# Kernel tuning notes

Hardware: AMD Instinct MI355X
Metric: run time of the kernel (lower is better)

## Reference

```python
import jax, jax.numpy as jnp
import numpy as np

B = 4096
SEQ = 128            # window_size * rnn_in_pkts
WINDOW = 32
IN_PKTS = 4
LEN_V, LEN_E = 1500, 64
IPD_V, IPD_E = 256, 64
EV = 64              # embedding_vector_bits
RNN_IN = IN_PKTS * EV   # 256
H = 256              # rnn_hidden_bits
LABELS = 100


def setup_inputs() -> dict:
    key = jax.random.key(0)
    ks = jax.random.split(key, 12)
    s = 0.05
    return {
        "len_x": jax.random.randint(ks[0], (B, SEQ), 0, LEN_V),
        "ipd_x": jax.random.randint(ks[1], (B, SEQ), 0, IPD_V),
        "len_emb": jax.random.normal(ks[2], (LEN_V, LEN_E), jnp.float32) * s,
        "ipd_emb": jax.random.normal(ks[3], (IPD_V, IPD_E), jnp.float32) * s,
        "fc_w": jax.random.normal(ks[4], (EV, LEN_E + IPD_E), jnp.float32) * s,
        "fc_b": jax.random.normal(ks[5], (EV,), jnp.float32) * s,
        "w_ih": jax.random.normal(ks[6], (3 * H, RNN_IN), jnp.float32) * s,
        "w_hh": jax.random.normal(ks[7], (3 * H, H), jnp.float32) * s,
        "b_ih": jax.random.normal(ks[8], (3 * H,), jnp.float32) * s,
        "b_hh": jax.random.normal(ks[9], (3 * H,), jnp.float32) * s,
        "out_w": jax.random.normal(ks[10], (LABELS, H), jnp.float32) * s,
        "out_b": jax.random.normal(ks[11], (LABELS,), jnp.float32) * s,
    }


def _gru_scan(rnn_in, w_ih, w_hh, b_ih, b_hh):
    # rnn_in: [B, T, RNN_IN]. Precompute input-side gates for all steps at once.
    gi_all = jnp.einsum("bti,gi->btg", rnn_in, w_ih) + b_ih  # [B,T,3H]
    h0 = jnp.zeros((rnn_in.shape[0], H), rnn_in.dtype)

    def step(h, gi):
        gh = h @ w_hh.T + b_hh                 # [B,3H]
        i_r, i_z, i_n = jnp.split(gi, 3, axis=-1)
        h_r, h_z, h_n = jnp.split(gh, 3, axis=-1)
        r = jax.nn.sigmoid(i_r + h_r)
        z = jax.nn.sigmoid(i_z + h_z)
        n = jnp.tanh(i_n + r * h_n)
        h_new = (1.0 - z) * n + z * h
        return h_new, None

    h_final, _ = jax.lax.scan(step, h0, jnp.swapaxes(gi_all, 0, 1))
    return h_final


def reference(len_x, ipd_x, len_emb, ipd_emb, fc_w, fc_b, w_ih, w_hh, b_ih, b_hh, out_w, out_b):
    len_e = len_emb[len_x]                      # [B,SEQ,LEN_E]
    ipd_e = ipd_emb[ipd_x]                      # [B,SEQ,IPD_E]
    cat = jnp.concatenate([len_e, ipd_e], axis=-1)
    evs = cat @ fc_w.T + fc_b                   # [B,SEQ,EV]
    rnn_in = evs.reshape(B, WINDOW, RNN_IN)     # [B,32,256]
    h = _gru_scan(rnn_in, w_ih, w_hh, b_ih, b_hh)
    logits = h @ out_w.T + out_b                # [B,LABELS]
    return logits
```

## Files before the change

kernel.cpp:

```cpp
#include <hip/hip_runtime.h>
#include <hip/hip_bf16.h>

typedef __bf16 bf16_t;
typedef __bf16 bf16x8 __attribute__((ext_vector_type(8)));
typedef float f32x4 __attribute__((ext_vector_type(4)));
typedef unsigned short u16x4 __attribute__((ext_vector_type(4)));

#define MFMA16(a, b, c) __builtin_amdgcn_mfma_f32_16x16x32_bf16((a), (b), (c), 0, 0, 0)

#define BATCH 4096
#define SEQN 128
#define HN 256
#define NLABELS 100
#define TSTEPS 32
#define LEN_VN 1500
#define IPD_VN 256

#define OFF_LENT   0u
#define OFF_IPDT   384000u
#define OFF_WIH    449536u
#define OFF_WHH    842752u
#define OFF_GI     1235968u
#define WS_NEEDED  202562560u

__device__ __forceinline__ float sigf(float x) {
    return __builtin_amdgcn_rcpf(1.f + __expf(-x));
}
__device__ __forceinline__ float tanh_fast(float x) {
    return 2.f * __builtin_amdgcn_rcpf(1.f + __expf(-2.f * x)) - 1.f;
}
__device__ __forceinline__ float b2f(unsigned short v) {
    union { unsigned u; float f; } c; c.u = ((unsigned)v) << 16; return c.f;
}
__device__ __forceinline__ unsigned short f2b(float f) {
    union { bf16_t h; unsigned short s; } c; c.h = (bf16_t)f; return c.s;
}

__device__ __forceinline__ void barrier_lds() {
    asm volatile("s_waitcnt lgkmcnt(0)\n\ts_barrier" ::: "memory");
}

__global__ void prep_kernel(const float* __restrict__ len_emb,
                            const float* __restrict__ ipd_emb,
                            const float* __restrict__ fc_w,
                            const float* __restrict__ fc_b,
                            const float* __restrict__ w_ih,
                            const float* __restrict__ w_hh,
                            float* __restrict__ lenT, float* __restrict__ ipdT,
                            bf16_t* __restrict__ wfrag_ih,
                            bf16_t* __restrict__ wfrag_hh) {
    const int bid = blockIdx.x, tid = threadIdx.x;
    if (bid < 439) {
        const int row = bid * 4 + (tid >> 6);
        const int e = tid & 63;
        if (row < LEN_VN) {
            const float* emb = len_emb + row * 64;
            const float* wv = fc_w + e * 128;
            float s = fc_b[e];
            #pragma unroll 8
            for (int j = 0; j < 64; ++j) s += emb[j] * wv[j];
            lenT[row * 64 + e] = s;
        } else if (row < LEN_VN + IPD_VN) {
            const int v = row - LEN_VN;
            const float* emb = ipd_emb + v * 64;
            const float* wv = fc_w + e * 128 + 64;
            float s = 0.f;
            #pragma unroll 8
            for (int j = 0; j < 64; ++j) s += emb[j] * wv[j];
            ipdT[v * 64 + e] = s;
        }
    } else {
        const int flat = (bid - 439) * 256 + tid;
        const int which = flat / 24576;
        const int rem = flat % 24576;
        const int c = rem >> 9;
        const int kt = (rem >> 6) & 7;
        const int lane = rem & 63;
        const int g = c * 16 + (lane & 15);
        const int k0 = kt * 32 + (lane >> 4) * 8;
        const float* src = (which == 0 ? w_ih : w_hh) + g * 256 + k0;
        bf16_t* dst = (which == 0 ? wfrag_ih : wfrag_hh) + ((c * 8 + kt) * 64 + lane) * 8;
        f32x4 s0 = *(const f32x4*)(src);
        f32x4 s1 = *(const f32x4*)(src + 4);
        bf16x8 o;
        #pragma unroll
        for (int j = 0; j < 4; ++j) { o[j] = (bf16_t)s0[j]; o[4 + j] = (bf16_t)s1[j]; }
        *(bf16x8*)dst = o;
    }
}

__global__ void __launch_bounds__(1024, 4)
gemm_gi(const int* __restrict__ len_x, const int* __restrict__ ipd_x,
        const float* __restrict__ lenT, const float* __restrict__ ipdT,
        const bf16_t* __restrict__ wfrag_ih,
        const float* __restrict__ b_ih, const float* __restrict__ b_hh,
        bf16_t* __restrict__ gi) {
    __shared__ bf16_t wlds[16 * 8 * 512];
    __shared__ bf16_t a_lds[2][8 * 512];

    const int tid = threadIdx.x;
    const int lane = tid & 63;
    const int w = tid >> 6;
    const int bt = blockIdx.x;
    const int col = lane & 15;

    bf16x8 wr[2][8];
    #pragma unroll
    for (int cc = 0; cc < 2; ++cc) {
        const int ct = cc * 16 + w;
        #pragma unroll
        for (int kt = 0; kt < 8; ++kt)
            wr[cc][kt] = *(const bf16x8*)(wfrag_ih + ((ct * 8 + kt) * 64 + lane) * 8);
    }
    #pragma unroll
    for (int kt = 0; kt < 8; ++kt)
        *(bf16x8*)&wlds[(w * 8 + kt) * 512 + lane * 8] =
            *(const bf16x8*)(wfrag_ih + (((32 + w) * 8 + kt) * 64 + lane) * 8);

    float bias0 = b_ih[w * 16 + col] + b_hh[w * 16 + col];
    float bias1 = b_ih[256 + w * 16 + col] + b_hh[256 + w * 16 + col];
    float bias2 = b_ih[512 + w * 16 + col];

    const int b_row = bt * 16 + (lane & 15);
    const int gkt = (tid >> 6) & 7;
    const int k0 = gkt * 32 + (lane >> 4) * 8;
    const int p = k0 >> 6;
    const int e0 = k0 & 63;

    auto do_gather = [&](int t) {
        const int seq = t * 4 + p;
        const int v1 = len_x[b_row * SEQN + seq];
        const int v2 = ipd_x[b_row * SEQN + seq];
        const f32x4* lp = (const f32x4*)(lenT + v1 * 64 + e0);
        const f32x4* ip = (const f32x4*)(ipdT + v2 * 64 + e0);
        f32x4 a0 = lp[0] + ip[0];
        f32x4 a1 = lp[1] + ip[1];
        bf16x8 o;
        #pragma unroll
        for (int j = 0; j < 4; ++j) { o[j] = (bf16_t)a0[j]; o[4 + j] = (bf16_t)a1[j]; }
        *(bf16x8*)&a_lds[t & 1][gkt * 512 + lane * 8] = o;
    };

    if (tid < 512) do_gather(0);
    bf16_t* gib = gi + (size_t)bt * 48 * 32 * 256 + lane * 4;
    const bf16_t* wb = &wlds[w * 8 * 512 + lane * 8];

    for (int t = 0; t < TSTEPS; ++t) {
        barrier_lds();
        if (t + 1 < TSTEPS && tid < 512) do_gather(t + 1);

        f32x4 acc0 = {}, acc1 = {}, acc2 = {};
        const bf16_t* ab = &a_lds[t & 1][lane * 8];
        #pragma unroll
        for (int kt = 0; kt < 8; ++kt) {
            bf16x8 af = *(const bf16x8*)(ab + kt * 512);
            bf16x8 w5 = *(const bf16x8*)(wb + kt * 512);
            acc0 = MFMA16(af, wr[0][kt], acc0);
            acc1 = MFMA16(af, wr[1][kt], acc1);
            acc2 = MFMA16(af, w5, acc2);
        }

        u16x4 o0, o1, o2;
        #pragma unroll
        for (int r = 0; r < 4; ++r) {
            o0[r] = f2b(acc0[r] + bias0);
            o1[r] = f2b(acc1[r] + bias1);
            o2[r] = f2b(acc2[r] + bias2);
        }
        *(u16x4*)(gib + ((size_t)(w) * 32 + t) * 256) = o0;
        *(u16x4*)(gib + ((size_t)(16 + w) * 32 + t) * 256) = o1;
        *(u16x4*)(gib + ((size_t)(32 + w) * 32 + t) * 256) = o2;
    }
}

__global__ void __launch_bounds__(1024, 4)
gru_kernel(const bf16_t* __restrict__ gi,
           const bf16_t* __restrict__ wfrag_hh,
           const float* __restrict__ b_hh,
           const float* __restrict__ out_w,
           const float* __restrict__ out_b,
           float* __restrict__ out) {
    __shared__ char smem[147456];
    bf16_t* wlds = (bf16_t*)smem;
    bf16_t* h_lds = (bf16_t*)(smem + 131072);
    float* h_fin = (float*)smem;

    const int tid = threadIdx.x;
    const int lane = tid & 63;
    const int w = tid >> 6;
    const int bt = blockIdx.x;
    const int col = lane & 15;
    const int j = w * 16 + col;

    bf16x8 wr[2][8];
    #pragma unroll
    for (int cc = 0; cc < 2; ++cc) {
        const int ct = cc * 16 + w;
        #pragma unroll
        for (int kt = 0; kt < 8; ++kt)
            wr[cc][kt] = *(const bf16x8*)(wfrag_hh + ((ct * 8 + kt) * 64 + lane) * 8);
    }
    #pragma unroll
    for (int kt = 0; kt < 8; ++kt)
        *(bf16x8*)&wlds[(w * 8 + kt) * 512 + lane * 8] =
            *(const bf16x8*)(wfrag_hh + (((32 + w) * 8 + kt) * 64 + lane) * 8);

    const float b_hn = b_hh[512 + j];

    for (int i = tid; i < 4096; i += 1024) h_lds[4096 + i] = (bf16_t)0.f;

    const int woff = (j >> 5) * 512 + (((j >> 3) & 3) * 16 + (lane >> 4) * 4) * 8 + (j & 7);

    f32x4 hprev = {};
    const bf16_t* gib = gi + (size_t)bt * 48 * 32 * 256 + lane * 4;
    const bf16_t* wb = &wlds[w * 8 * 512 + lane * 8];

    for (int t = 0; t < TSTEPS; ++t) {
        barrier_lds();

        u16x4 g0 = *(const u16x4*)(gib + ((size_t)(w) * 32 + t) * 256);
        u16x4 g1 = *(const u16x4*)(gib + ((size_t)(16 + w) * 32 + t) * 256);
        u16x4 g2 = *(const u16x4*)(gib + ((size_t)(32 + w) * 32 + t) * 256);

        const bf16_t* hb = &h_lds[((t + 1) & 1) * 4096 + lane * 8];
        f32x4 acc0 = {}, acc1 = {}, acc2 = {};
        #pragma unroll
        for (int kt = 0; kt < 8; ++kt) {
            bf16x8 ah = *(const bf16x8*)(hb + kt * 512);
            bf16x8 w5 = *(const bf16x8*)(wb + kt * 512);
            acc0 = MFMA16(ah, wr[0][kt], acc0);
            acc1 = MFMA16(ah, wr[1][kt], acc1);
            acc2 = MFMA16(ah, w5, acc2);
        }

        bf16_t* hw = &h_lds[(t & 1) * 4096 + woff];
        #pragma unroll
        for (int r = 0; r < 4; ++r) {
            float rg = sigf(acc0[r] + b2f(g0[r]));
            float zg = sigf(acc1[r] + b2f(g1[r]));
            float ng = tanh_fast(b2f(g2[r]) + rg * (acc2[r] + b_hn));
            float hn = ng + zg * (hprev[r] - ng);
            hprev[r] = hn;
            hw[r * 8] = (bf16_t)hn;
        }
    }

    __syncthreads();

    #pragma unroll
    for (int r = 0; r < 4; ++r) {
        const int m = (lane >> 4) * 4 + r;
        h_fin[m * 260 + j] = hprev[r];
    }
    __syncthreads();

    for (int i = tid; i < 16 * NLABELS; i += 1024) {
        const int row = i / NLABELS;
        const int cl = i - row * NLABELS;
        const f32x4* wrow = (const f32x4*)(out_w + cl * 256);
        const f32x4* hr = (const f32x4*)(h_fin + row * 260);
        f32x4 acc = {0.f, 0.f, 0.f, 0.f};
        #pragma unroll 4
        for (int k = 0; k < 64; ++k) acc += hr[k] * wrow[k];
        out[(bt * 16 + row) * NLABELS + cl] =
            out_b[cl] + acc[0] + acc[1] + acc[2] + acc[3];
    }
}

extern "C" void kernel_launch(void* const* d_in, const int* in_sizes, int n_in,
                              void* d_out, int out_size, void* d_ws, size_t ws_size,
                              hipStream_t stream) {
    (void)in_sizes; (void)n_in; (void)out_size; (void)ws_size;
    const int*   len_x   = (const int*)d_in[0];
    const int*   ipd_x   = (const int*)d_in[1];
    const float* len_emb = (const float*)d_in[2];
    const float* ipd_emb = (const float*)d_in[3];
    const float* fc_w    = (const float*)d_in[4];
    const float* fc_b    = (const float*)d_in[5];
    const float* w_ih    = (const float*)d_in[6];
    const float* w_hh    = (const float*)d_in[7];
    const float* b_ih    = (const float*)d_in[8];
    const float* b_hh    = (const float*)d_in[9];
    const float* out_w   = (const float*)d_in[10];
    const float* out_b   = (const float*)d_in[11];

    char* ws = (char*)d_ws;
    float*  lenT = (float*)(ws + OFF_LENT);
    float*  ipdT = (float*)(ws + OFF_IPDT);
    bf16_t* wfi  = (bf16_t*)(ws + OFF_WIH);
    bf16_t* wfh  = (bf16_t*)(ws + OFF_WHH);
    bf16_t* gi   = (bf16_t*)(ws + OFF_GI);

    prep_kernel<<<631, 256, 0, stream>>>(len_emb, ipd_emb, fc_w, fc_b,
                                         w_ih, w_hh, lenT, ipdT, wfi, wfh);
    gemm_gi<<<256, 1024, 0, stream>>>(len_x, ipd_x, lenT, ipdT, wfi,
                                      b_ih, b_hh, gi);
    gru_kernel<<<256, 1024, 0, stream>>>(gi, wfh, b_hh, out_w, out_b,
                                         (float*)d_out);
}
```

Baseline: 249.7 us.

## Halve block size, give each wave two column tiles per gate

Both the input-gate GEMM and the GRU recurrence kernels now launch 512-thread blocks instead of 1024. Each wave owns two 16-column tiles per gate, six accumulators in total, with five tiles held in registers and one in LDS. The MFMA operands are swapped so the weights act as the A operand, which yields a transposed output layout. Hidden-state writes and biases become vectorized 4-wide. The intent is to cut LDS footprint and per-step barrier cost across fewer waves while raising MFMA work per wave, at the price of much higher register pressure.

New measurement: 263.9 us. 1.06x slower.

```diff
diff --git a/kernel.cpp b/kernel.cpp
--- a/kernel.cpp
+++ b/kernel.cpp
@@ -89,41 +89,44 @@
     }
 }
 
-__global__ void __launch_bounds__(1024, 4)
+__global__ void __launch_bounds__(512, 2)
 gemm_gi(const int* __restrict__ len_x, const int* __restrict__ ipd_x,
         const float* __restrict__ lenT, const float* __restrict__ ipdT,
         const bf16_t* __restrict__ wfrag_ih,
         const float* __restrict__ b_ih, const float* __restrict__ b_hh,
         bf16_t* __restrict__ gi) {
-    __shared__ bf16_t wlds[16 * 8 * 512];
+    __shared__ bf16_t wlds[8 * 8 * 512];
     __shared__ bf16_t a_lds[2][8 * 512];
 
     const int tid = threadIdx.x;
     const int lane = tid & 63;
     const int w = tid >> 6;
     const int bt = blockIdx.x;
-    const int col = lane & 15;
-
-    bf16x8 wr[2][8];
-    #pragma unroll
-    for (int cc = 0; cc < 2; ++cc) {
-        const int ct = cc * 16 + w;
+    const int quad = lane >> 4;
+
+    const int cts[6] = {2*w, 2*w + 1, 16 + 2*w, 17 + 2*w, 32 + 2*w, 33 + 2*w};
+
+    bf16x8 wr[5][8];
+    #pragma unroll
+    for (int cc = 0; cc < 5; ++cc)
         #pragma unroll
         for (int kt = 0; kt < 8; ++kt)
-            wr[cc][kt] = *(const bf16x8*)(wfrag_ih + ((ct * 8 + kt) * 64 + lane) * 8);
-    }
+            wr[cc][kt] = *(const bf16x8*)(wfrag_ih + ((cts[cc] * 8 + kt) * 64 + lane) * 8);
     #pragma unroll
     for (int kt = 0; kt < 8; ++kt)
         *(bf16x8*)&wlds[(w * 8 + kt) * 512 + lane * 8] =
-            *(const bf16x8*)(wfrag_ih + (((32 + w) * 8 + kt) * 64 + lane) * 8);
-
-    float bias0 = b_ih[w * 16 + col] + b_hh[w * 16 + col];
-    float bias1 = b_ih[256 + w * 16 + col] + b_hh[256 + w * 16 + col];
-    float bias2 = b_ih[512 + w * 16 + col];
+            *(const bf16x8*)(wfrag_ih + ((cts[5] * 8 + kt) * 64 + lane) * 8);
+
+    f32x4 bias[6];
+    #pragma unroll
+    for (int cc = 0; cc < 6; ++cc) {
+        f32x4 v = *(const f32x4*)(b_ih + cts[cc] * 16 + quad * 4);
+        if (cc < 4) v += *(const f32x4*)(b_hh + cts[cc] * 16 + quad * 4);
+        bias[cc] = v;
+    }
 
     const int b_row = bt * 16 + (lane & 15);
-    const int gkt = (tid >> 6) & 7;
-    const int k0 = gkt * 32 + (lane >> 4) * 8;
+    const int k0 = w * 32 + quad * 8;
     const int p = k0 >> 6;
     const int e0 = k0 & 63;
 
@@ -138,123 +141,135 @@
         bf16x8 o;
         #pragma unroll
         for (int j = 0; j < 4; ++j) { o[j] = (bf16_t)a0[j]; o[4 + j] = (bf16_t)a1[j]; }
-        *(bf16x8*)&a_lds[t & 1][gkt * 512 + lane * 8] = o;
+        *(bf16x8*)&a_lds[t & 1][w * 512 + lane * 8] = o;
     };
 
-    if (tid < 512) do_gather(0);
+    do_gather(0);
     bf16_t* gib = gi + (size_t)bt * 48 * 32 * 256 + lane * 4;
     const bf16_t* wb = &wlds[w * 8 * 512 + lane * 8];
 
     for (int t = 0; t < TSTEPS; ++t) {
         barrier_lds();
-        if (t + 1 < TSTEPS && tid < 512) do_gather(t + 1);
-
-        f32x4 acc0 = {}, acc1 = {}, acc2 = {};
+        if (t + 1 < TSTEPS) do_gather(t + 1);
+
+        f32x4 acc[6] = {};
         const bf16_t* ab = &a_lds[t & 1][lane * 8];
         #pragma unroll
         for (int kt = 0; kt < 8; ++kt) {
-            bf16x8 af = *(const bf16x8*)(ab + kt * 512);
+            bf16x8 xf = *(const bf16x8*)(ab + kt * 512);
             bf16x8 w5 = *(const bf16x8*)(wb + kt * 512);
-            acc0 = MFMA16(af, wr[0][kt], acc0);
-            acc1 = MFMA16(af, wr[1][kt], acc1);
-            acc2 = MFMA16(af, w5, acc2);
-        }
-
-        u16x4 o0, o1, o2;
-        #pragma unroll
-        for (int r = 0; r < 4; ++r) {
-            o0[r] = f2b(acc0[r] + bias0);
-            o1[r] = f2b(acc1[r] + bias1);
-            o2[r] = f2b(acc2[r] + bias2);
-        }
-        *(u16x4*)(gib + ((size_t)(w) * 32 + t) * 256) = o0;
-        *(u16x4*)(gib + ((size_t)(16 + w) * 32 + t) * 256) = o1;
-        *(u16x4*)(gib + ((size_t)(32 + w) * 32 + t) * 256) = o2;
-    }
-}
-
-__global__ void __launch_bounds__(1024, 4)
+            acc[0] = MFMA16(wr[0][kt], xf, acc[0]);
+            acc[1] = MFMA16(wr[1][kt], xf, acc[1]);
+            acc[2] = MFMA16(wr[2][kt], xf, acc[2]);
+            acc[3] = MFMA16(wr[3][kt], xf, acc[3]);
+            acc[4] = MFMA16(wr[4][kt], xf, acc[4]);
+            acc[5] = MFMA16(w5, xf, acc[5]);
+        }
+
+        #pragma unroll
+        for (int cc = 0; cc < 6; ++cc) {
+            u16x4 o;
+            #pragma unroll
+            for (int r = 0; r < 4; ++r) o[r] = f2b(acc[cc][r] + bias[cc][r]);
+            *(u16x4*)(gib + ((size_t)cts[cc] * 32 + t) * 256) = o;
+        }
+    }
+}
+
+__global__ void __launch_bounds__(512, 2)
 gru_kernel(const bf16_t* __restrict__ gi,
            const bf16_t* __restrict__ wfrag_hh,
            const float* __restrict__ b_hh,
            const float* __restrict__ out_w,
            const float* __restrict__ out_b,
            float* __restrict__ out) {
-    __shared__ char smem[147456];
+    __shared__ char smem[81920];
     bf16_t* wlds = (bf16_t*)smem;
-    bf16_t* h_lds = (bf16_t*)(smem + 131072);
+    bf16_t* h_lds = (bf16_t*)(smem + 65536);
     float* h_fin = (float*)smem;
 
     const int tid = threadIdx.x;
     const int lane = tid & 63;
     const int w = tid >> 6;
     const int bt = blockIdx.x;
-    const int col = lane & 15;
-    const int j = w * 16 + col;
-
-    bf16x8 wr[2][8];
-    #pragma unroll
-    for (int cc = 0; cc < 2; ++cc) {
-        const int ct = cc * 16 + w;
+    const int quad = lane >> 4;
+    const int b = lane & 15;
+
+    const int cts[6] = {2*w, 2*w + 1, 16 + 2*w, 17 + 2*w, 32 + 2*w, 33 + 2*w};
+
+    bf16x8 wr[5][8];
+    #pragma unroll
+    for (int cc = 0; cc < 5; ++cc)
         #pragma unroll
         for (int kt = 0; kt < 8; ++kt)
-            wr[cc][kt] = *(const bf16x8*)(wfrag_hh + ((ct * 8 + kt) * 64 + lane) * 8);
-    }
+            wr[cc][kt] = *(const bf16x8*)(wfrag_hh + ((cts[cc] * 8 + kt) * 64 + lane) * 8);
     #pragma unroll
     for (int kt = 0; kt < 8; ++kt)
         *(bf16x8*)&wlds[(w * 8 + kt) * 512 + lane * 8] =
-            *(const bf16x8*)(wfrag_hh + (((32 + w) * 8 + kt) * 64 + lane) * 8);
-
-    const float b_hn = b_hh[512 + j];
-
-    for (int i = tid; i < 4096; i += 1024) h_lds[4096 + i] = (bf16_t)0.f;
-
-    const int woff = (j >> 5) * 512 + (((j >> 3) & 3) * 16 + (lane >> 4) * 4) * 8 + (j & 7);
-
-    f32x4 hprev = {};
+            *(const bf16x8*)(wfrag_hh + ((cts[5] * 8 + kt) * 64 + lane) * 8);
+
+    f32x4 bhn[2];
+    bhn[0] = *(const f32x4*)(b_hh + cts[4] * 16 + quad * 4);
+    bhn[1] = *(const f32x4*)(b_hh + cts[5] * 16 + quad * 4);
+
+    for (int i = tid; i < 4096; i += 512) h_lds[4096 + i] = (bf16_t)0.f;
+
+    int woff[2];
+    #pragma unroll
+    for (int s = 0; s < 2; ++s)
+        woff[s] = w * 512 + (((2 * s + (quad >> 1)) & 3) * 16 + b) * 8 + 4 * (quad & 1);
+
+    f32x4 hprev[2] = {};
     const bf16_t* gib = gi + (size_t)bt * 48 * 32 * 256 + lane * 4;
     const bf16_t* wb = &wlds[w * 8 * 512 + lane * 8];
 
     for (int t = 0; t < TSTEPS; ++t) {
         barrier_lds();
 
-        u16x4 g0 = *(const u16x4*)(gib + ((size_t)(w) * 32 + t) * 256);
-        u16x4 g1 = *(const u16x4*)(gib + ((size_t)(16 + w) * 32 + t) * 256);
-        u16x4 g2 = *(const u16x4*)(gib + ((size_t)(32 + w) * 32 + t) * 256);
+        u16x4 g[6];
+        #pragma unroll
+        for (int cc = 0; cc < 6; ++cc)
+            g[cc] = *(const u16x4*)(gib + ((size_t)cts[cc] * 32 + t) * 256);
 
         const bf16_t* hb = &h_lds[((t + 1) & 1) * 4096 + lane * 8];
-        f32x4 acc0 = {}, acc1 = {}, acc2 = {};
+        f32x4 acc[6] = {};
         #pragma unroll
         for (int kt = 0; kt < 8; ++kt) {
-            bf16x8 ah = *(const bf16x8*)(hb + kt * 512);
+            bf16x8 hf = *(const bf16x8*)(hb + kt * 512);
             bf16x8 w5 = *(const bf16x8*)(wb + kt * 512);
-            acc0 = MFMA16(ah, wr[0][kt], acc0);
-            acc1 = MFMA16(ah, wr[1][kt], acc1);
-            acc2 = MFMA16(ah, w5, acc2);
-        }
-
-        bf16_t* hw = &h_lds[(t & 1) * 4096 + woff];
-        #pragma unroll
-        for (int r = 0; r < 4; ++r) {
-            float rg = sigf(acc0[r] + b2f(g0[r]));
-            float zg = sigf(acc1[r] + b2f(g1[r]));
-            float ng = tanh_fast(b2f(g2[r]) + rg * (acc2[r] + b_hn));
-            float hn = ng + zg * (hprev[r] - ng);
-            hprev[r] = hn;
-            hw[r * 8] = (bf16_t)hn;
+            acc[0] = MFMA16(wr[0][kt], hf, acc[0]);
+            acc[1] = MFMA16(wr[1][kt], hf, acc[1]);
+            acc[2] = MFMA16(wr[2][kt], hf, acc[2]);
+            acc[3] = MFMA16(wr[3][kt], hf, acc[3]);
+            acc[4] = MFMA16(wr[4][kt], hf, acc[4]);
+            acc[5] = MFMA16(w5, hf, acc[5]);
+        }
+
+        bf16_t* hwb = &h_lds[(t & 1) * 4096];
+        #pragma unroll
+        for (int s = 0; s < 2; ++s) {
+            u16x4 o;
+            #pragma unroll
+            for (int r = 0; r < 4; ++r) {
+                float rg = sigf(acc[s][r] + b2f(g[s][r]));
+                float zg = sigf(acc[2 + s][r] + b2f(g[2 + s][r]));
+                float ng = tanh_fast(b2f(g[4 + s][r]) + rg * (acc[4 + s][r] + bhn[s][r]));
+                float hn = ng + zg * (hprev[s][r] - ng);
+                hprev[s][r] = hn;
+                o[r] = f2b(hn);
+            }
+            *(u16x4*)(hwb + woff[s]) = o;
         }
     }
 
     __syncthreads();
 
     #pragma unroll
-    for (int r = 0; r < 4; ++r) {
-        const int m = (lane >> 4) * 4 + r;
-        h_fin[m * 260 + j] = hprev[r];
-    }
+    for (int s = 0; s < 2; ++s)
+        *(f32x4*)(h_fin + b * 260 + 32 * w + 16 * s + 4 * quad) = hprev[s];
     __syncthreads();
 
-    for (int i = tid; i < 16 * NLABELS; i += 1024) {
+    for (int i = tid; i < 16 * NLABELS; i += 512) {
         const int row = i / NLABELS;
         const int cl = i - row * NLABELS;
         const f32x4* wrow = (const f32x4*)(out_w + cl * 256);
@@ -293,8 +308,8 @@
 
     prep_kernel<<<631, 256, 0, stream>>>(len_emb, ipd_emb, fc_w, fc_b,
                                          w_ih, w_hh, lenT, ipdT, wfi, wfh);
-    gemm_gi<<<256, 1024, 0, stream>>>(len_x, ipd_x, lenT, ipdT, wfi,
-                                      b_ih, b_hh, gi);
-    gru_kernel<<<256, 1024, 0, stream>>>(gi, wfh, b_hh, out_w, out_b,
-                                         (float*)d_out);
-}
+    gemm_gi<<<256, 512, 0, stream>>>(len_x, ipd_x, lenT, ipdT, wfi,
+                                     b_ih, b_hh, gi);
+    gru_kernel<<<256, 512, 0, stream>>>(gi, wfh, b_hh, out_w, out_b,
+                                        (float*)d_out);
+}
```
